# Kernel tuning notes

Hardware: AMD Instinct MI355X
Metric: run time of the kernel (lower is better)

Reference implementation:

```python
import jax, jax.numpy as jnp
import numpy as np

# PSLoss constants (from init_kwargs)
MSE_WEIGHT = 0.5
W_CORR = 1.0
W_VAR = 1.0
W_MEAN = 1.0
K = 3           # k_dominant_freqs
MIN_PATCH = 5   # min_patch_len (max(2, 5))
EPS = 1e-8


def setup_inputs() -> dict:
    key = jax.random.key(0)
    k1, k2 = jax.random.split(key)
    B, T, F = 64, 336, 321
    forecast = jax.random.normal(k1, (B, T, F), dtype=jnp.float32)
    target = jax.random.normal(k2, (B, T, F), dtype=jnp.float32)
    return {"forecast": forecast, "target": target}


def _structural_loss(fc, tg):
    """fc, tg: [N, T] flattened (batch*features) series. Returns (total_loss_sum, patch_count)."""
    N, T = tg.shape
    Mmax = T // MIN_PATCH  # max segments per period (period >= MIN_PATCH)

    # --- Fourier adaptive patching (vectorized over all N series) ---
    amp = jnp.abs(jnp.fft.rfft(tg, axis=-1))[:, 1:]           # drop DC, [N, T//2]
    _, rel = jax.lax.top_k(amp, K)                             # [N, K]
    freq_idx = (rel + 1).astype(jnp.float32)
    p = jnp.floor(T / freq_idx).astype(jnp.int32)              # dominant periods [N, K]
    # dedup periods in topk order (the original 'processed_periods' set)
    eq = p[:, :, None] == p[:, None, :]                        # [N, K, K]
    earlier = jnp.tril(jnp.ones((K, K), dtype=bool), -1)       # j < k
    dup = jnp.any(eq & earlier, axis=-1)
    valid_p = (p >= MIN_PATCH) & ~dup                          # [N, K]

    nseg = T // p                                              # [N, K] (p >= 2 always)
    s_idx = jnp.arange(Mmax, dtype=jnp.int32)
    seg_s = p[:, :, None] * s_idx                              # [N, K, Mmax]
    seg_e = seg_s + p[:, :, None]
    seg_v = (s_idx < nseg[:, :, None]) & valid_p[:, :, None]
    rem_s = nseg * p                                           # remaining tail patch
    rem_v = valid_p & ((T - rem_s) >= MIN_PATCH)

    starts = jnp.concatenate([seg_s.reshape(N, -1), rem_s], axis=-1)
    ends = jnp.concatenate([seg_e.reshape(N, -1), jnp.full_like(rem_s, T)], axis=-1)
    valid = jnp.concatenate([seg_v.reshape(N, -1), rem_v], axis=-1)
    # fallback whole-series patch if no patch survived
    none = ~jnp.any(valid, axis=-1, keepdims=True)
    starts = jnp.concatenate([starts, jnp.zeros((N, 1), jnp.int32)], axis=-1)
    ends = jnp.concatenate([ends, jnp.full((N, 1), T, jnp.int32)], axis=-1)
    valid = jnp.concatenate([valid, none], axis=-1)            # [N, M]

    # --- dedup identical (start, end) patches (original list(set(...))) ---
    SENT = (T + 1) * (T + 1)
    keys = jnp.where(valid, starts * (T + 1) + ends, SENT)
    keys = jnp.sort(keys, axis=-1)
    uniq = jnp.concatenate(
        [jnp.ones((N, 1), dtype=bool), keys[:, 1:] != keys[:, :-1]], axis=-1)
    valid = (keys != SENT) & uniq
    s = jnp.where(valid, keys // (T + 1), 0)                   # safe dummy (0,2) when invalid
    e = jnp.where(valid, keys % (T + 1), 2)

    # --- per-patch stats via inclusive prefix sums ---
    def csum(x):
        return jnp.concatenate([jnp.zeros((N, 1), x.dtype), jnp.cumsum(x, axis=-1)], axis=-1)

    cs_t, cs_f = csum(tg), csum(fc)
    cs_tt, cs_ff, cs_tf = csum(tg * tg), csum(fc * fc), csum(tg * fc)

    def seg_sum(cs):
        return jnp.take_along_axis(cs, e, axis=-1) - jnp.take_along_axis(cs, s, axis=-1)

    n = (e - s).astype(jnp.float32)
    St, Sf = seg_sum(cs_t), seg_sum(cs_f)
    Stt, Sff, Stf = seg_sum(cs_tt), seg_sum(cs_ff), seg_sum(cs_tf)
    mt, mf = St / n, Sf / n
    tvs = jnp.maximum(Stt - n * mt * mt, 0.0)   # sum of squared deviations (target)
    fvs = jnp.maximum(Sff - n * mf * mf, 0.0)
    num = Stf - n * mt * mf
    corr = num / (jnp.sqrt(tvs * fvs) + EPS)
    corr_loss = 1.0 - jnp.abs(corr)
    tvar = tvs / (n - 1.0)                      # torch.var is unbiased
    fvar = fvs / (n - 1.0)
    var_loss = jnp.abs(tvar - fvar) / (tvar + EPS)
    mean_loss = jnp.abs(mt - mf) / (jnp.abs(mt) + EPS)
    patch_loss = W_CORR * corr_loss + W_VAR * var_loss + W_MEAN * mean_loss

    total = jnp.sum(jnp.where(valid, patch_loss, 0.0))
    count = jnp.sum(valid)
    return total, count


def reference(forecast, target):
    B, T, F = forecast.shape
    fc = jnp.transpose(forecast, (0, 2, 1)).reshape(B * F, T)
    tg = jnp.transpose(target, (0, 2, 1)).reshape(B * F, T)
    total, count = _structural_loss(fc, tg)
    avg = jnp.where(count > 0,
                    total / jnp.maximum(count, 1).astype(jnp.float32),
                    jnp.float32(0.0))
    mse = jnp.mean((forecast - target) ** 2)
    return MSE_WEIGHT * mse + (1.0 - MSE_WEIGHT) * avg
```

## Files before the change

### kernel.cpp

```cpp
#include <hip/hip_runtime.h>
#include <hip/hip_bf16.h>

#define TT 336
#define NF 321
#define NB 64
#define NSER (NB * NF)
#define WPB 4
#define KP 352
#define LDA 360
#define SPP 16
#define NFB (NSER / SPP)
#define NFBG 1288
#define TSP 340
#define TBL 337

#define TGX 11
#define TGY 11
#define NMSEP (TGX * TGY * NB)

typedef __attribute__((ext_vector_type(8))) short bf16x8;
typedef __attribute__((ext_vector_type(4))) float f32x4;
typedef unsigned long long ULL;

__device__ __forceinline__ unsigned short f2bf(float v) {
    unsigned x = __float_as_uint(v);
    x += 0x7FFFu + ((x >> 16) & 1u);
    return (unsigned short)(x >> 16);
}

__device__ __forceinline__ void ins3(ULL& a0, ULL& a1, ULL& a2, ULL x) {
    ULL hi = a0 > x ? a0 : x;
    ULL lo = a0 > x ? x : a0;
    a0 = hi;
    ULL hi1 = a1 > lo ? a1 : lo;
    ULL lo1 = a1 > lo ? lo : a1;
    a1 = hi1;
    a2 = a2 > lo1 ? a2 : lo1;
}

__device__ __forceinline__ int idiv336(int d) {
    return (int)(__fdividef(336.0f, (float)d));
}

__global__ void twiddle_k(unsigned short* __restrict__ Wb) {
    int n = blockIdx.x;
    int f = (n >> 1) + 1;
    int isSin = n & 1;
    for (int k = threadIdx.x; k < KP; k += blockDim.x) {
        float v = 0.0f;
        if (k < TT) {
            int r = (f * k) % TT;
            float ang = 6.2831853071795864769f * (float)r / 336.0f;
            v = isSin ? sinf(ang) : cosf(ang);
        }
        Wb[(size_t)n * KP + k] = f2bf(v);
    }
}

__device__ __forceinline__ float patch_loss_f32(float S1, float S2, float S3,
                                                float S4, float S5, int n) {
    float nnf = (float)n;
    float invf = 1.0f / nnf;
    float tvs = S3 - S1 * S1 * invf; tvs = tvs > 0.f ? tvs : 0.f;
    float fvs = S4 - S2 * S2 * invf; fvs = fvs > 0.f ? fvs : 0.f;
    float num = S5 - S1 * S2 * invf;
    float corr = num / (sqrtf(tvs * fvs) + 1e-8f);
    float closs = 1.0f - fabsf(corr);
    float vloss = fabsf(tvs - fvs) / (tvs + (nnf - 1.0f) * 1e-8f);
    float mloss = fabsf(S1 - S2) / (fabsf(S1) + nnf * 1e-8f);
    return closs + vloss + mloss;
}

__device__ __forceinline__ double patch_loss(double S1, double S2, double S3,
                                             double S4, double S5, double nn) {
    double mt = S1 / nn, mf = S2 / nn;
    double tvs = S3 - nn * mt * mt; tvs = tvs > 0.0 ? tvs : 0.0;
    double fvs = S4 - nn * mf * mf; fvs = fvs > 0.0 ? fvs : 0.0;
    double num = S5 - nn * mt * mf;
    double corr = num / (sqrt(tvs * fvs) + 1e-8);
    double closs = 1.0 - fabs(corr);
    double tvar = tvs / (nn - 1.0), fvar = fvs / (nn - 1.0);
    double vloss = fabs(tvar - fvar) / (tvar + 1e-8);
    double mloss = fabs(mt - mf) / (fabs(mt) + 1e-8);
    return closs + vloss + mloss;
}

struct PatchCfg {
    int P[3], nseg[3], rs[3];
    bool vp[3], hr[3];
};

__device__ __forceinline__ void make_cfg(int fr0, int fr1, int fr2, PatchCfg& c) {
    c.P[0] = idiv336(fr0); c.P[1] = idiv336(fr1); c.P[2] = idiv336(fr2);
    c.vp[0] = (c.P[0] >= 5);
    c.vp[1] = (c.P[1] >= 5) && (c.P[1] != c.P[0]);
    c.vp[2] = (c.P[2] >= 5) && (c.P[2] != c.P[0]) && (c.P[2] != c.P[1]);
#pragma unroll
    for (int q = 0; q < 3; q++) {
        c.nseg[q] = idiv336(c.P[q] > 0 ? c.P[q] : 1);
        c.rs[q] = c.nseg[q] * c.P[q];
        c.hr[q] = c.vp[q] && ((TT - c.rs[q]) >= 5);
    }
}

__device__ __forceinline__ bool slot_patch(const PatchCfg& c, int i, int& s, int& e) {
    bool kept = false;
    s = 0; e = 0;
    if (i < 204) {
        int k = (i >= 136) ? 2 : ((i >= 68) ? 1 : 0);
        int si = i - k * 68;
        if (c.vp[k]) {
            if (si < c.nseg[k]) { s = c.P[k] * si; e = s + c.P[k]; kept = true; }
            else if (si == c.nseg[k] && c.hr[k]) { s = c.rs[k]; e = TT; kept = true; }
            if (kept) {
#pragma unroll
                for (int j = 0; j < 2; j++) {
                    if (j < k && c.vp[j]) {
                        bool dup = (s == c.rs[j]) && (e == TT) && c.hr[j];
                        int len = e - s;
                        if (len == c.P[j] && s < c.rs[j] && (s % c.P[j]) == 0) dup = true;
                        if (dup) kept = false;
                    }
                }
            }
        }
    }
    return kept;
}

__global__ __launch_bounds__(256) void fused_k(const float* __restrict__ tgO,
                                               const float* __restrict__ fcO,
                                               const unsigned short* __restrict__ Wb,
                                               double* __restrict__ blkout) {
    __shared__ __align__(16) char smem[43520 + 26960];
    float2* ts = (float2*)smem;
    unsigned short* sA = (unsigned short*)(smem + 43520);
    ULL* tk3 = (ULL*)(smem + 43520 + 11520);
    float* tabW = (float*)(smem + 43520);
    __shared__ uint4 tkf[SPP];
    __shared__ double wms[4], wls[4];
    __shared__ int wlc[4];

    const int tid = threadIdx.x;
    const int wave = tid >> 6, lane = tid & 63;
    const int lb = (blockIdx.x & 7) * 161 + (blockIdx.x >> 3);
    if (lb >= NFB) return;
    const int serBase = lb * SPP;

    {
        const int j = tid & 15, tch = tid >> 4;
        const int ser = serBase + j;
        const int bb = ser / NF, ff = ser - bb * NF;
        const float* tb_ = tgO + (size_t)bb * TT * NF + ff;
        const float* fb_ = fcO + (size_t)bb * TT * NF + ff;
        const int t0 = tch * 21;
        float va[21], vc[21];
#pragma unroll
        for (int i = 0; i < 21; i++) va[i] = tb_[(size_t)(t0 + i) * NF];
#pragma unroll
        for (int i = 0; i < 21; i++) vc[i] = fb_[(size_t)(t0 + i) * NF];
        float ms = 0.0f;
#pragma unroll
        for (int i = 0; i < 21; i++) {
            int t = t0 + i;
            ts[j * TSP + t] = make_float2(va[i], vc[i]);
            sA[j * LDA + t] = f2bf(va[i]);
            float d = va[i] - vc[i];
            ms = fmaf(d, d, ms);
        }
        for (int off = 32; off; off >>= 1) ms += __shfl_down(ms, off, 64);
        if (lane == 0) wms[wave] = (double)ms;
        sA[(tid & 15) * LDA + TT + (tid >> 4)] = 0;
    }
    __syncthreads();

    {
        const int quad = lane >> 4, c = lane & 15;
        const unsigned short* aRow = sA + c * LDA + quad * 8;
        const int ntStart = wave * 5;
        const int ntEnd = (wave == 3) ? 21 : ntStart + 5;

        ULL t0k[4] = {0, 0, 0, 0}, t1k[4] = {0, 0, 0, 0}, t2k[4] = {0, 0, 0, 0};
        for (int nt = ntStart; nt < ntEnd; nt++) {
            const unsigned short* bRow = Wb + (size_t)(nt * 16 + c) * KP + quad * 8;
            f32x4 acc = (f32x4){0.f, 0.f, 0.f, 0.f};
#pragma unroll
            for (int ks = 0; ks < 11; ks++) {
                bf16x8 a = *(const bf16x8*)(aRow + ks * 32);
                bf16x8 b = *(const bf16x8*)(bRow + ks * 32);
                acc = __builtin_amdgcn_mfma_f32_16x16x32_bf16(a, b, acc, 0, 0, 0);
            }
            int n = nt * 16 + c;
            unsigned fidx = (unsigned)((n >> 1) + 1);
            unsigned ftag = 0xFFFFFFFFu - fidx;
            bool odd = (n & 1) != 0;
#pragma unroll
            for (int r = 0; r < 4; r++) {
                float v = acc[r];
                float p = v * v;
                p += __shfl_xor(p, 1, 64);
                ULL key = odd ? 0ull
                              : (((ULL)__float_as_uint(p) << 32) | (ULL)ftag);
                ins3(t0k[r], t1k[r], t2k[r], key);
            }
        }
#pragma unroll
        for (int m = 2; m <= 8; m <<= 1) {
#pragma unroll
            for (int r = 0; r < 4; r++) {
                ULL b0 = __shfl_xor(t0k[r], m, 64);
                ULL b1 = __shfl_xor(t1k[r], m, 64);
                ULL b2 = __shfl_xor(t2k[r], m, 64);
                ins3(t0k[r], t1k[r], t2k[r], b0);
                ins3(t0k[r], t1k[r], t2k[r], b1);
                ins3(t0k[r], t1k[r], t2k[r], b2);
            }
        }
        if (c == 0) {
#pragma unroll
            for (int r = 0; r < 4; r++) {
                int s = quad * 4 + r;
                tk3[(wave * 16 + s) * 3 + 0] = t0k[r];
                tk3[(wave * 16 + s) * 3 + 1] = t1k[r];
                tk3[(wave * 16 + s) * 3 + 2] = t2k[r];
            }
        }
    }
    __syncthreads();
    if (tid < SPP) {
        ULL k0 = 0, k1 = 0, k2 = 0;
#pragma unroll
        for (int wv = 0; wv < 4; wv++) {
#pragma unroll
            for (int j = 0; j < 3; j++) ins3(k0, k1, k2, tk3[(wv * 16 + tid) * 3 + j]);
        }
        unsigned f0 = 0xFFFFFFFFu - (unsigned)(k0 & 0xFFFFFFFFull);
        unsigned f1 = 0xFFFFFFFFu - (unsigned)(k1 & 0xFFFFFFFFull);
        unsigned f2 = 0xFFFFFFFFu - (unsigned)(k2 & 0xFFFFFFFFull);
        tkf[tid] = make_uint4(f0, f1, f2, 0u);
    }
    __syncthreads();

    float* tw = tabW + wave * (5 * TBL);
    float lsum = 0.0f;
    int lcnt = 0;
#pragma unroll 1
    for (int r = 0; r < 4; r++) {
        const int jj = (wave << 2) | r;

        float2 loc[6];
        float c1 = 0.f, c2 = 0.f, c3 = 0.f, c4 = 0.f, c5 = 0.f;
        if (lane < 56) {
            const float4* lp = (const float4*)(ts + jj * TSP + 6 * lane);
            float4 va = lp[0], vb = lp[1], vcc = lp[2];
            loc[0] = make_float2(va.x, va.y); loc[1] = make_float2(va.z, va.w);
            loc[2] = make_float2(vb.x, vb.y); loc[3] = make_float2(vb.z, vb.w);
            loc[4] = make_float2(vcc.x, vcc.y); loc[5] = make_float2(vcc.z, vcc.w);
#pragma unroll
            for (int i = 0; i < 6; i++) {
                float a = loc[i].x, b = loc[i].y;
                c1 += a; c2 += b;
                c3 = fmaf(a, a, c3); c4 = fmaf(b, b, c4); c5 = fmaf(a, b, c5);
            }
        }

        float s1 = c1, s2 = c2, s3 = c3, s4 = c4, s5 = c5;
#pragma unroll
        for (int off = 1; off < 64; off <<= 1) {
            float y1 = __shfl_up(s1, off, 64);
            float y2 = __shfl_up(s2, off, 64);
            float y3 = __shfl_up(s3, off, 64);
            float y4 = __shfl_up(s4, off, 64);
            float y5 = __shfl_up(s5, off, 64);
            if (lane >= off) { s1 += y1; s2 += y2; s3 += y3; s4 += y4; s5 += y5; }
        }

        if (lane == 63) {
            tw[0 * TBL] = 0.f; tw[1 * TBL] = 0.f; tw[2 * TBL] = 0.f;
            tw[3 * TBL] = 0.f; tw[4 * TBL] = 0.f;
        }
        if (lane < 56) {
            float r1 = s1 - c1, r2 = s2 - c2;
            float r3 = s3 - c3, r4 = s4 - c4, r5 = s5 - c5;
#pragma unroll
            for (int i = 0; i < 6; i++) {
                float a = loc[i].x, b = loc[i].y;
                r1 += a; r2 += b;
                r3 = fmaf(a, a, r3); r4 = fmaf(b, b, r4); r5 = fmaf(a, b, r5);
                int ix = 6 * lane + i + 1;
                tw[0 * TBL + ix] = r1; tw[1 * TBL + ix] = r2;
                tw[2 * TBL + ix] = r3; tw[3 * TBL + ix] = r4; tw[4 * TBL + ix] = r5;
            }
        }

        uint4 tk = tkf[jj];
        PatchCfg cfg;
        make_cfg((int)tk.x, (int)tk.y, (int)tk.z, cfg);

        ULL anyMask = 0ull;
#pragma unroll
        for (int rI = 0; rI < 4; rI++) {
            int s, e;
            bool kept = slot_patch(cfg, lane + 64 * rI, s, e);
            ULL bal = __ballot(kept);
            anyMask |= bal;
            if (bal == 0ull) continue;
            if (kept) {
                float S1 = tw[0 * TBL + e] - tw[0 * TBL + s];
                float S2 = tw[1 * TBL + e] - tw[1 * TBL + s];
                float S3 = tw[2 * TBL + e] - tw[2 * TBL + s];
                float S4 = tw[3 * TBL + e] - tw[3 * TBL + s];
                float S5 = tw[4 * TBL + e] - tw[4 * TBL + s];
                lsum += patch_loss_f32(S1, S2, S3, S4, S5, e - s);
                lcnt += 1;
            }
        }
        if (anyMask == 0ull) {
            if (lane == 0) {
                lsum += patch_loss_f32(tw[0 * TBL + TT], tw[1 * TBL + TT],
                                       tw[2 * TBL + TT], tw[3 * TBL + TT],
                                       tw[4 * TBL + TT], TT);
                lcnt += 1;
            }
        }
    }

    for (int off = 32; off; off >>= 1) {
        lsum += __shfl_down(lsum, off, 64);
        lcnt += __shfl_down(lcnt, off, 64);
    }
    if (lane == 0) { wls[wave] = (double)lsum; wlc[wave] = lcnt; }
    __syncthreads();
    if (tid == 0) {
        blkout[3 * lb + 0] = wls[0] + wls[1] + wls[2] + wls[3];
        blkout[3 * lb + 1] = (double)(wlc[0] + wlc[1] + wlc[2] + wlc[3]);
        blkout[3 * lb + 2] = wms[0] + wms[1] + wms[2] + wms[3];
    }
}

__global__ __launch_bounds__(256) void transpose_k(const float* __restrict__ fc,
                                                   const float* __restrict__ tg,
                                                   float2* __restrict__ out,
                                                   double* __restrict__ msep,
                                                   double* __restrict__ acc) {
    __shared__ float ta[32][33];
    __shared__ float tb[32][33];
    __shared__ double wacc[4];
    const int b = blockIdx.z;
    const int t0 = blockIdx.x * 32, f0 = blockIdx.y * 32;
    const int tx = threadIdx.x, ty = threadIdx.y;
    const size_t base = (size_t)b * TT * NF;
    double ms = 0.0;
#pragma unroll
    for (int k = 0; k < 4; k++) {
        int t = t0 + ty + 8 * k, f = f0 + tx;
        if (t < TT && f < NF) {
            float a = tg[base + (size_t)t * NF + f];
            float c = fc[base + (size_t)t * NF + f];
            ta[ty + 8 * k][tx] = a;
            tb[ty + 8 * k][tx] = c;
            double d = (double)a - (double)c;
            ms += d * d;
        }
    }
    __syncthreads();
#pragma unroll
    for (int k = 0; k < 4; k++) {
        int f = f0 + ty + 8 * k, t = t0 + tx;
        if (t < TT && f < NF) {
            out[((size_t)b * NF + f) * TT + t] =
                make_float2(ta[tx][ty + 8 * k], tb[tx][ty + 8 * k]);
        }
    }
    for (int off = 32; off; off >>= 1) ms += __shfl_down(ms, off, 64);
    int flat = ty * 32 + tx;
    int lane = flat & 63, wid = flat >> 6;
    if (lane == 0) wacc[wid] = ms;
    __syncthreads();
    if (flat == 0) {
        double tot = wacc[0] + wacc[1] + wacc[2] + wacc[3];
        if (msep) {
            int blk = (blockIdx.z * TGY + blockIdx.y) * TGX + blockIdx.x;
            msep[blk] = tot;
        } else {
            atomicAdd(&acc[0], tot);
        }
    }
}

__global__ void mse_k(const float* __restrict__ fc, const float* __restrict__ tg,
                      double* __restrict__ acc) {
    const size_t N4 = (size_t)NB * TT * NF / 4;
    const float4* a4 = (const float4*)fc;
    const float4* b4 = (const float4*)tg;
    double s = 0.0;
    for (size_t i = (size_t)blockIdx.x * blockDim.x + threadIdx.x; i < N4;
         i += (size_t)gridDim.x * blockDim.x) {
        float4 a = a4[i], b = b4[i];
        double d0 = (double)a.x - (double)b.x;
        double d1 = (double)a.y - (double)b.y;
        double d2 = (double)a.z - (double)b.z;
        double d3 = (double)a.w - (double)b.w;
        s += d0 * d0 + d1 * d1 + d2 * d2 + d3 * d3;
    }
    for (int off = 32; off; off >>= 1) s += __shfl_down(s, off, 64);
    __shared__ double wsum[4];
    int flat = threadIdx.x;
    int lane = flat & 63, wid = flat >> 6;
    if (lane == 0) wsum[wid] = s;
    __syncthreads();
    if (flat == 0) atomicAdd(&acc[0], wsum[0] + wsum[1] + wsum[2] + wsum[3]);
}

__device__ __forceinline__ void patch_body(const float2* tsw, int lane,
                                           int fr0, int fr1, int fr2,
                                           double& lsum, double& lcnt) {
    PatchCfg cfg;
    make_cfg(fr0, fr1, fr2, cfg);
    ULL anyMask = 0ull;
#pragma unroll
    for (int rI = 0; rI < 4; rI++) {
        int s, e;
        bool kept = slot_patch(cfg, lane + 64 * rI, s, e);
        anyMask |= __ballot(kept);
        if (kept) {
            double S1 = 0, S2 = 0, S3 = 0, S4 = 0, S5 = 0;
            for (int t = s; t < e; t++) {
                float2 v = tsw[t];
                double a = (double)v.x, b = (double)v.y;
                S1 += a; S2 += b;
                S3 += a * a; S4 += b * b; S5 += a * b;
            }
            lsum += patch_loss(S1, S2, S3, S4, S5, (double)(e - s));
            lcnt += 1.0;
        }
    }
    if (anyMask == 0ull) {
        double S1 = 0, S2 = 0, S3 = 0, S4 = 0, S5 = 0;
        for (int t = lane; t < TT; t += 64) {
            float2 v = tsw[t];
            double a = (double)v.x, b = (double)v.y;
            S1 += a; S2 += b;
            S3 += a * a; S4 += b * b; S5 += a * b;
        }
        for (int off = 32; off; off >>= 1) {
            S1 += __shfl_down(S1, off, 64);
            S2 += __shfl_down(S2, off, 64);
            S3 += __shfl_down(S3, off, 64);
            S4 += __shfl_down(S4, off, 64);
            S5 += __shfl_down(S5, off, 64);
        }
        if (lane == 0) {
            lsum += patch_loss(S1, S2, S3, S4, S5, (double)TT);
            lcnt += 1.0;
        }
    }
}

__global__ __launch_bounds__(256, 6) void series_k(const float2* __restrict__ tsG,
                                                   const float* __restrict__ fcG,
                                                   const float* __restrict__ tgG,
                                                   int transposed,
                                                   double2* __restrict__ pairs,
                                                   double* __restrict__ acc) {
    const int w = threadIdx.x >> 6, lane = threadIdx.x & 63;
    const int ser = blockIdx.x * WPB + w;
    __shared__ float2 ts[WPB][TT];
    __shared__ float4 zb[WPB][84];

    if (transposed) {
        const float2* sp = tsG + (size_t)ser * TT;
        for (int t = lane; t < TT; t += 64) ts[w][t] = sp[t];
    } else {
        int b = ser / NF, f = ser - b * NF;
        const float* tp = tgG + (size_t)b * TT * NF + f;
        const float* fp = fcG + (size_t)b * TT * NF + f;
        for (int t = lane; t < TT; t += 64)
            ts[w][t] = make_float2(tp[(size_t)t * NF], fp[(size_t)t * NF]);
    }
    __syncthreads();

    for (int t = lane; t < 84; t += 64) {
        float x0 = ts[w][t].x, x1 = ts[w][t + 84].x;
        float x2 = ts[w][t + 168].x, x3 = ts[w][t + 252].x;
        float a = x0 + x2, b2 = x1 + x3, c = x0 - x2, d = x1 - x3;
        zb[w][t] = make_float4(a + b2, a - b2, c, d);
    }
    __syncthreads();

    const double TWOPI = 6.283185307179586476925286766559;
    int fb[3] = {1 + lane, 65 + lane, 129 + lane};
    float cc[3], sn[3], re[3], im[3], cd[3], sd[3], sgn[3];
    int selA[3];
#pragma unroll
    for (int q = 0; q < 3; q++) {
        int f = fb[q], cls = f & 3;
        double dl = (double)f * (TWOPI / 336.0);
        cd[q] = (float)cos(dl);
        sd[q] = (float)sin(dl);
        cc[q] = 1.0f; sn[q] = 0.0f; re[q] = 0.0f; im[q] = 0.0f;
        sgn[q] = (cls == 1) ? -1.0f : ((cls == 3) ? 1.0f : 0.0f);
        selA[q] = (cls == 0) ? 0 : ((cls == 2) ? 1 : 2);
    }
    for (int t = 0; t < 84; t++) {
        float4 zv = zb[w][t];
#pragma unroll
        for (int q = 0; q < 3; q++) {
            float zr = (selA[q] == 0) ? zv.x : ((selA[q] == 1) ? zv.y : zv.z);
            float zi = sgn[q] * zv.w;
            re[q] = fmaf(zr, cc[q], re[q]);
            re[q] = fmaf(zi, sn[q], re[q]);
            im[q] = fmaf(zi, cc[q], im[q]);
            im[q] = fmaf(-zr, sn[q], im[q]);
            float nc = fmaf(cc[q], cd[q], -(sn[q] * sd[q]));
            float ns = fmaf(sn[q], cd[q], cc[q] * sd[q]);
            cc[q] = nc; sn[q] = ns;
        }
    }

    ULL k0 = 0, k1 = 0, k2 = 0;
#pragma unroll
    for (int q = 0; q < 3; q++) {
        float a2 = fmaf(re[q], re[q], im[q] * im[q]);
        ULL key = ((ULL)__float_as_uint(a2) << 32) |
                  (ULL)(0xFFFFFFFFu - (unsigned)fb[q]);
        if (fb[q] > 168) key = 0ull;
        ins3(k0, k1, k2, key);
    }
    for (int m = 1; m < 64; m <<= 1) {
        ULL b0 = __shfl_xor(k0, m, 64);
        ULL b1 = __shfl_xor(k1, m, 64);
        ULL b2 = __shfl_xor(k2, m, 64);
        ins3(k0, k1, k2, b0); ins3(k0, k1, k2, b1); ins3(k0, k1, k2, b2);
    }

    int fr0 = (int)(0xFFFFFFFFu - (unsigned)(k0 & 0xFFFFFFFFull));
    int fr1 = (int)(0xFFFFFFFFu - (unsigned)(k1 & 0xFFFFFFFFull));
    int fr2 = (int)(0xFFFFFFFFu - (unsigned)(k2 & 0xFFFFFFFFull));

    double lsum = 0.0, lcnt = 0.0;
    patch_body(&ts[w][0], lane, fr0, fr1, fr2, lsum, lcnt);

    for (int off = 32; off; off >>= 1) {
        lsum += __shfl_down(lsum, off, 64);
        lcnt += __shfl_down(lcnt, off, 64);
    }
    if (lane == 0) {
        if (pairs) {
            pairs[ser] = make_double2(lsum, lcnt);
        } else {
            atomicAdd(&acc[1], lsum);
            atomicAdd(&acc[2], lcnt);
        }
    }
}

__global__ __launch_bounds__(1024) void reduce3_k(const double* __restrict__ blkout,
                                                  float* __restrict__ out) {
    const int tid = threadIdx.x;
    double ls = 0.0, lc = 0.0, ms = 0.0;
    for (int i = tid; i < NFB; i += 1024) {
        ls += blkout[3 * i + 0];
        lc += blkout[3 * i + 1];
        ms += blkout[3 * i + 2];
    }
    for (int off = 32; off; off >>= 1) {
        ls += __shfl_down(ls, off, 64);
        lc += __shfl_down(lc, off, 64);
        ms += __shfl_down(ms, off, 64);
    }
    __shared__ double sl[16], sc[16], sm[16];
    int lane = tid & 63, wid = tid >> 6;
    if (lane == 0) { sl[wid] = ls; sc[wid] = lc; sm[wid] = ms; }
    __syncthreads();
    if (tid == 0) {
        double L = 0, C = 0, M = 0;
        for (int i = 0; i < 16; i++) { L += sl[i]; C += sc[i]; M += sm[i]; }
        double mse = M / (double)((size_t)NB * TT * NF);
        double avg = (C > 0.0) ? (L / C) : 0.0;
        out[0] = (float)(0.5 * mse + 0.5 * avg);
    }
}

__global__ __launch_bounds__(1024) void reduce_k(const double2* __restrict__ pairs,
                                                 const double* __restrict__ msep,
                                                 int nmse,
                                                 float* __restrict__ out) {
    const int tid = threadIdx.x;
    double ls = 0.0, lc = 0.0, ms = 0.0;
    for (int i = tid; i < NSER; i += 1024) {
        double2 p = pairs[i];
        ls += p.x; lc += p.y;
    }
    for (int i = tid; i < nmse; i += 1024) ms += msep[i];
    for (int off = 32; off; off >>= 1) {
        ls += __shfl_down(ls, off, 64);
        lc += __shfl_down(lc, off, 64);
        ms += __shfl_down(ms, off, 64);
    }
    __shared__ double sl[16], sc[16], sm[16];
    int lane = tid & 63, wid = tid >> 6;
    if (lane == 0) { sl[wid] = ls; sc[wid] = lc; sm[wid] = ms; }
    __syncthreads();
    if (tid == 0) {
        double L = 0, C = 0, M = 0;
        for (int i = 0; i < 16; i++) { L += sl[i]; C += sc[i]; M += sm[i]; }
        double mse = M / (double)((size_t)NB * TT * NF);
        double avg = (C > 0.0) ? (L / C) : 0.0;
        out[0] = (float)(0.5 * mse + 0.5 * avg);
    }
}

__global__ void finalize_k(const double* __restrict__ acc, float* __restrict__ out) {
    double mse = acc[0] / (double)((size_t)NB * TT * NF);
    double avg = (acc[2] > 0.0) ? (acc[1] / acc[2]) : 0.0;
    out[0] = (float)(0.5 * mse + 0.5 * avg);
}

extern "C" void kernel_launch(void* const* d_in, const int* in_sizes, int n_in,
                              void* d_out, int out_size, void* d_ws, size_t ws_size,
                              hipStream_t stream) {
    const float* fc = (const float*)d_in[0];
    const float* tg = (const float*)d_in[1];
    float* out = (float*)d_out;
    char* ws = (char*)d_ws;
    double* acc = (double*)ws;

    const size_t OFF_MSE = 64;
    const size_t OFF_PAIR = OFF_MSE + (size_t)NMSEP * sizeof(double);
    const size_t OFF_TOP = OFF_PAIR + (size_t)NSER * sizeof(double2);
    const size_t OFF_W = OFF_TOP + (size_t)NSER * sizeof(uint4);
    const size_t OFF_END2 = OFF_W + (size_t)TT * KP * sizeof(unsigned short);
    const size_t bytesT = (size_t)NSER * TT * sizeof(float2);
    const bool big2 = (ws_size >= OFF_END2);
    const size_t R3_OFF_TS = OFF_PAIR + (size_t)NSER * sizeof(double2);
    const bool big = !big2 && (ws_size >= R3_OFF_TS + bytesT);
    const bool mid = !big2 && !big && (ws_size >= OFF_MSE + bytesT);

    double* msep = (double*)(ws + OFF_MSE);
    double* blkout = (double*)(ws + OFF_PAIR);
    unsigned short* Wb = (unsigned short*)(ws + OFF_W);

    dim3 tg_grid(TGX, TGY, NB);
    dim3 tg_blk(32, 8);

    if (big2) {
        twiddle_k<<<TT, 128, 0, stream>>>(Wb);
        fused_k<<<NFBG, 256, 0, stream>>>(tg, fc, Wb, blkout);
        reduce3_k<<<1, 1024, 0, stream>>>(blkout, out);
    } else if (big) {
        float2* tsT = (float2*)(ws + R3_OFF_TS);
        transpose_k<<<tg_grid, tg_blk, 0, stream>>>(fc, tg, tsT, msep, acc);
        series_k<<<NSER / WPB, 64 * WPB, 0, stream>>>(tsT, fc, tg, 1,
                                                      (double2*)blkout, acc);
        reduce_k<<<1, 1024, 0, stream>>>((double2*)blkout, msep, NMSEP, out);
    } else if (mid) {
        float2* tsT = (float2*)(ws + OFF_MSE);
        hipMemsetAsync(d_ws, 0, 64, stream);
        transpose_k<<<tg_grid, tg_blk, 0, stream>>>(fc, tg, tsT, nullptr, acc);
        series_k<<<NSER / WPB, 64 * WPB, 0, stream>>>(tsT, fc, tg, 1, nullptr, acc);
        finalize_k<<<1, 1, 0, stream>>>(acc, out);
    } else {
        hipMemsetAsync(d_ws, 0, 64, stream);
        mse_k<<<1024, 256, 0, stream>>>(fc, tg, acc);
        series_k<<<NSER / WPB, 64 * WPB, 0, stream>>>(nullptr, fc, tg, 0, nullptr, acc);
        finalize_k<<<1, 1, 0, stream>>>(acc, out);
    }
}
```

Measured before the change: 152.8 us.

## Double waves per block in fused kernel and store only boundary prefix sums

The fused kernel now launches 8 waves per block instead of 4. Load work, MFMA column tiles and per-series patch evaluation are redistributed so each wave handles 2 series instead of 4. To fit eight per-wave tables in shared memory, the full 336-entry prefix-sum table is replaced by a compact table. It keeps only prefix values at multiples of each dominant period plus the series end, found with a float reciprocal test. This aims to raise parallelism and latency hiding per block, at the cost of more shared memory per block, extra index arithmetic, and a float-rounding dependence in the period-multiple test.

```diff
diff --git a/kernel.cpp b/kernel.cpp
--- a/kernel.cpp
+++ b/kernel.cpp
@@ -9,10 +9,12 @@
 #define KP 352
 #define LDA 360
 #define SPP 16
+#define WV 8
 #define NFB (NSER / SPP)
 #define NFBG 1288
 #define TSP 340
-#define TBL 337
+
+#define TWS 1056
 
 #define TGX 11
 #define TGY 11
@@ -87,6 +89,7 @@
 
 struct PatchCfg {
     int P[3], nseg[3], rs[3];
+    float rp[3];
     bool vp[3], hr[3];
 };
 
@@ -100,6 +103,7 @@
         c.nseg[q] = idiv336(c.P[q] > 0 ? c.P[q] : 1);
         c.rs[q] = c.nseg[q] * c.P[q];
         c.hr[q] = c.vp[q] && ((TT - c.rs[q]) >= 5);
+        c.rp[q] = (c.P[q] > 0) ? __frcp_rn((float)c.P[q]) : 0.0f;
     }
 }
 
@@ -128,18 +132,18 @@
     return kept;
 }
 
-__global__ __launch_bounds__(256) void fused_k(const float* __restrict__ tgO,
+__global__ __launch_bounds__(512) void fused_k(const float* __restrict__ tgO,
                                                const float* __restrict__ fcO,
                                                const unsigned short* __restrict__ Wb,
                                                double* __restrict__ blkout) {
-    __shared__ __align__(16) char smem[43520 + 26960];
+    __shared__ __align__(16) char smem[43520 + WV * TWS * 4];
     float2* ts = (float2*)smem;
     unsigned short* sA = (unsigned short*)(smem + 43520);
     ULL* tk3 = (ULL*)(smem + 43520 + 11520);
-    float* tabW = (float*)(smem + 43520);
+    float* tabAll = (float*)(smem + 43520);
     __shared__ uint4 tkf[SPP];
-    __shared__ double wms[4], wls[4];
-    __shared__ int wlc[4];
+    __shared__ double wms[WV], wls[WV];
+    __shared__ int wlc[WV];
 
     const int tid = threadIdx.x;
     const int wave = tid >> 6, lane = tid & 63;
@@ -153,32 +157,36 @@
         const int bb = ser / NF, ff = ser - bb * NF;
         const float* tb_ = tgO + (size_t)bb * TT * NF + ff;
         const float* fb_ = fcO + (size_t)bb * TT * NF + ff;
-        const int t0 = tch * 21;
-        float va[21], vc[21];
-#pragma unroll
-        for (int i = 0; i < 21; i++) va[i] = tb_[(size_t)(t0 + i) * NF];
-#pragma unroll
-        for (int i = 0; i < 21; i++) vc[i] = fb_[(size_t)(t0 + i) * NF];
+        int t0, nT;
+        if (tch < 16) { t0 = tch * 11; nT = 11; }
+        else          { t0 = 176 + (tch - 16) * 10; nT = 10; }
+        float va[11], vc[11];
+#pragma unroll
+        for (int i = 0; i < 11; i++) if (i < nT) va[i] = tb_[(size_t)(t0 + i) * NF];
+#pragma unroll
+        for (int i = 0; i < 11; i++) if (i < nT) vc[i] = fb_[(size_t)(t0 + i) * NF];
         float ms = 0.0f;
 #pragma unroll
-        for (int i = 0; i < 21; i++) {
-            int t = t0 + i;
-            ts[j * TSP + t] = make_float2(va[i], vc[i]);
-            sA[j * LDA + t] = f2bf(va[i]);
-            float d = va[i] - vc[i];
-            ms = fmaf(d, d, ms);
+        for (int i = 0; i < 11; i++) {
+            if (i < nT) {
+                int t = t0 + i;
+                ts[j * TSP + t] = make_float2(va[i], vc[i]);
+                sA[j * LDA + t] = f2bf(va[i]);
+                float d = va[i] - vc[i];
+                ms = fmaf(d, d, ms);
+            }
         }
         for (int off = 32; off; off >>= 1) ms += __shfl_down(ms, off, 64);
         if (lane == 0) wms[wave] = (double)ms;
-        sA[(tid & 15) * LDA + TT + (tid >> 4)] = 0;
+        if (tid < SPP * 16) sA[(tid & 15) * LDA + TT + (tid >> 4)] = 0;
     }
     __syncthreads();
 
     {
         const int quad = lane >> 4, c = lane & 15;
         const unsigned short* aRow = sA + c * LDA + quad * 8;
-        const int ntStart = wave * 5;
-        const int ntEnd = (wave == 3) ? 21 : ntStart + 5;
+        const int ntStart = (wave < 5) ? wave * 3 : 15 + (wave - 5) * 2;
+        const int ntEnd = ntStart + ((wave < 5) ? 3 : 2);
 
         ULL t0k[4] = {0, 0, 0, 0}, t1k[4] = {0, 0, 0, 0}, t2k[4] = {0, 0, 0, 0};
         for (int nt = ntStart; nt < ntEnd; nt++) {
@@ -230,7 +238,7 @@
     if (tid < SPP) {
         ULL k0 = 0, k1 = 0, k2 = 0;
 #pragma unroll
-        for (int wv = 0; wv < 4; wv++) {
+        for (int wv = 0; wv < WV; wv++) {
 #pragma unroll
             for (int j = 0; j < 3; j++) ins3(k0, k1, k2, tk3[(wv * 16 + tid) * 3 + j]);
         }
@@ -241,12 +249,16 @@
     }
     __syncthreads();
 
-    float* tw = tabW + wave * (5 * TBL);
+    float* tw = tabAll + wave * TWS;
     float lsum = 0.0f;
     int lcnt = 0;
 #pragma unroll 1
-    for (int r = 0; r < 4; r++) {
-        const int jj = (wave << 2) | r;
+    for (int r = 0; r < 2; r++) {
+        const int jj = (wave << 1) | r;
+
+        uint4 tk = tkf[jj];
+        PatchCfg cfg;
+        make_cfg((int)tk.x, (int)tk.y, (int)tk.z, cfg);
 
         float2 loc[6];
         float c1 = 0.f, c2 = 0.f, c3 = 0.f, c4 = 0.f, c5 = 0.f;
@@ -276,8 +288,11 @@
         }
 
         if (lane == 63) {
-            tw[0 * TBL] = 0.f; tw[1 * TBL] = 0.f; tw[2 * TBL] = 0.f;
-            tw[3 * TBL] = 0.f; tw[4 * TBL] = 0.f;
+#pragma unroll
+            for (int k = 0; k < 3; k++) {
+#pragma unroll
+                for (int q = 0; q < 5; q++) tw[(k * 70) * 5 + q] = 0.f;
+            }
         }
         if (lane < 56) {
             float r1 = s1 - c1, r2 = s2 - c2;
@@ -287,39 +302,54 @@
                 float a = loc[i].x, b = loc[i].y;
                 r1 += a; r2 += b;
                 r3 = fmaf(a, a, r3); r4 = fmaf(b, b, r4); r5 = fmaf(a, b, r5);
-                int ix = 6 * lane + i + 1;
-                tw[0 * TBL + ix] = r1; tw[1 * TBL + ix] = r2;
-                tw[2 * TBL + ix] = r3; tw[3 * TBL + ix] = r4; tw[4 * TBL + ix] = r5;
-            }
-        }
-
-        uint4 tk = tkf[jj];
-        PatchCfg cfg;
-        make_cfg((int)tk.x, (int)tk.y, (int)tk.z, cfg);
+                int tp = 6 * lane + i + 1;
+                float tpf = (float)tp;
+                if (tp == TT) {
+                    tw[1050] = r1; tw[1051] = r2; tw[1052] = r3;
+                    tw[1053] = r4; tw[1054] = r5;
+                }
+#pragma unroll
+                for (int k = 0; k < 3; k++) {
+                    if (cfg.vp[k]) {
+                        int q = (int)(tpf * cfg.rp[k] + 0.001f);
+                        if (q * cfg.P[k] == tp && q <= 68) {
+                            int ix = (k * 70 + q) * 5;
+                            tw[ix + 0] = r1; tw[ix + 1] = r2; tw[ix + 2] = r3;
+                            tw[ix + 3] = r4; tw[ix + 4] = r5;
+                        }
+                    }
+                }
+            }
+        }
 
         ULL anyMask = 0ull;
 #pragma unroll
         for (int rI = 0; rI < 4; rI++) {
+            int i = lane + 64 * rI;
             int s, e;
-            bool kept = slot_patch(cfg, lane + 64 * rI, s, e);
+            bool kept = slot_patch(cfg, i, s, e);
             ULL bal = __ballot(kept);
             anyMask |= bal;
             if (bal == 0ull) continue;
             if (kept) {
-                float S1 = tw[0 * TBL + e] - tw[0 * TBL + s];
-                float S2 = tw[1 * TBL + e] - tw[1 * TBL + s];
-                float S3 = tw[2 * TBL + e] - tw[2 * TBL + s];
-                float S4 = tw[3 * TBL + e] - tw[3 * TBL + s];
-                float S5 = tw[4 * TBL + e] - tw[4 * TBL + s];
+                int k = (i >= 136) ? 2 : ((i >= 68) ? 1 : 0);
+                int si = i - k * 68;
+                bool tail = (si == cfg.nseg[k]);
+                const float* pS = tw + (k * 70 + si) * 5;
+                const float* pE = tail ? (tw + 1050) : (tw + (k * 70 + si + 1) * 5);
+                float S1 = pE[0] - pS[0];
+                float S2 = pE[1] - pS[1];
+                float S3 = pE[2] - pS[2];
+                float S4 = pE[3] - pS[3];
+                float S5 = pE[4] - pS[4];
                 lsum += patch_loss_f32(S1, S2, S3, S4, S5, e - s);
                 lcnt += 1;
             }
         }
         if (anyMask == 0ull) {
             if (lane == 0) {
-                lsum += patch_loss_f32(tw[0 * TBL + TT], tw[1 * TBL + TT],
-                                       tw[2 * TBL + TT], tw[3 * TBL + TT],
-                                       tw[4 * TBL + TT], TT);
+                lsum += patch_loss_f32(tw[1050], tw[1051], tw[1052],
+                                       tw[1053], tw[1054], TT);
                 lcnt += 1;
             }
         }
@@ -332,9 +362,13 @@
     if (lane == 0) { wls[wave] = (double)lsum; wlc[wave] = lcnt; }
     __syncthreads();
     if (tid == 0) {
-        blkout[3 * lb + 0] = wls[0] + wls[1] + wls[2] + wls[3];
-        blkout[3 * lb + 1] = (double)(wlc[0] + wlc[1] + wlc[2] + wlc[3]);
-        blkout[3 * lb + 2] = wms[0] + wms[1] + wms[2] + wms[3];
+        double L = 0.0, M = 0.0;
+        int C = 0;
+#pragma unroll
+        for (int wv = 0; wv < WV; wv++) { L += wls[wv]; C += wlc[wv]; M += wms[wv]; }
+        blkout[3 * lb + 0] = L;
+        blkout[3 * lb + 1] = (double)C;
+        blkout[3 * lb + 2] = M;
     }
 }
 
@@ -646,7 +680,7 @@
 
     if (big2) {
         twiddle_k<<<TT, 128, 0, stream>>>(Wb);
-        fused_k<<<NFBG, 256, 0, stream>>>(tg, fc, Wb, blkout);
+        fused_k<<<NFBG, 64 * WV, 0, stream>>>(tg, fc, Wb, blkout);
         reduce3_k<<<1, 1024, 0, stream>>>(blkout, out);
     } else if (big) {
         float2* tsT = (float2*)(ws + R3_OFF_TS);
```

Result: no change. 150.2 us (-1.7%).
